# Kernel tuning notes

Hardware: AMD Instinct MI355X
Metric: run time of the kernel (lower is better)

Reference implementation:

```python
import jax, jax.numpy as jnp
import numpy as np

EPS = 1e-6          # RMSNorm eps
SINK_EPS = 1e-12    # Sinkhorn denominator eps
N_ITER = 5          # sinkhorn_iters


def setup_inputs() -> dict:
    key = jax.random.key(0)
    ks = jax.random.split(key, 12)
    B, T, H, D = 2, 2048, 4, 2048
    FD = H * D
    W_SCALE = 0.02  # keep gate logits in a non-saturated sigmoid range
    return {
        "x": jax.random.normal(ks[0], (B, T, H, D), jnp.float32),
        "norm_w": jnp.ones((FD,), jnp.float32),
        "w_pre": jax.random.normal(ks[1], (H, FD), jnp.float32) * W_SCALE,
        "w_res": jax.random.normal(ks[2], (H * H, FD), jnp.float32) * W_SCALE,
        "w_post": jax.random.normal(ks[3], (H, FD), jnp.float32) * W_SCALE,
        "alpha_pre": jax.random.uniform(ks[4], (1,), jnp.float32),
        "alpha_res": jax.random.uniform(ks[5], (1,), jnp.float32),
        "alpha_post": jax.random.uniform(ks[6], (1,), jnp.float32),
        "s_pre": jax.random.normal(ks[7], (H,), jnp.float32),
        "s_res": jax.random.normal(ks[8], (H, H), jnp.float32),
        "s_post": jax.random.normal(ks[9], (H,), jnp.float32),
        "w_inner": jax.random.normal(ks[10], (D, D), jnp.float32) * (1.0 / np.sqrt(D)),
    }


def sinkhorn_knopp(logits, n_iter):
    # Doubly-stochastic projection over last two dims.
    m = jnp.exp(logits - jnp.max(logits, axis=(-2, -1), keepdims=True))
    for _ in range(n_iter):
        m = m / (jnp.sum(m, axis=-1, keepdims=True) + SINK_EPS)
        m = m / (jnp.sum(m, axis=-2, keepdims=True) + SINK_EPS)
    return m


def reference(x, norm_w, w_pre, w_res, w_post, alpha_pre, alpha_res, alpha_post,
              s_pre, s_res, s_post, w_inner):
    b, t, h, d = x.shape
    flat = x.reshape(b, t, h * d)
    # RMSNorm over flat dim
    var = jnp.mean(flat * flat, axis=-1, keepdims=True)
    normed = norm_w * flat * jax.lax.rsqrt(var + EPS)
    # Gate projections (Linear, no bias => x @ W.T)
    a_raw = alpha_pre * (normed @ w_pre.T) + s_pre                     # (b,t,h)
    b_raw = (alpha_res * (normed @ w_res.T)).reshape(b, t, h, h) + s_res
    c_raw = alpha_post * (normed @ w_post.T) + s_post                  # (b,t,h)
    a_l = jax.nn.sigmoid(a_raw)
    c_l = 2.0 * jax.nn.sigmoid(c_raw)
    b_l = sinkhorn_knopp(b_raw, N_ITER)
    # split: inner input
    inner_in = jnp.einsum('bth,bthd->btd', a_l, x)
    # inner layer: bias-free linear
    inner_out = inner_in @ w_inner.T
    # combine
    carry = jnp.einsum('bthk,btkd->bthd', b_l, x)
    write = jnp.einsum('bth,btd->bthd', c_l, inner_out)
    return carry + write
```

## Files before the change

### kernel.cpp

```cpp
#include <hip/hip_runtime.h>
#include <hip/hip_bf16.h>

#define FD 8192
#define DD 2048
#define NH 4
#define NT 4096
#define NG 24
#define NGP 32
#define KSPLIT 32
#define KC (FD / KSPLIT)
#define CH 64

typedef __attribute__((ext_vector_type(4))) float f32x4;
typedef __attribute__((ext_vector_type(8))) short short8;

__device__ inline unsigned short f2bf(float f) {
  __hip_bfloat16 h = __float2bfloat16(f);
  unsigned short u; __builtin_memcpy(&u, &h, 2); return u;
}
__device__ inline float bf2f(unsigned short u) {
  __hip_bfloat16 h; __builtin_memcpy(&h, &u, 2); return __bfloat162float(h);
}

__global__ __launch_bounds__(256) void k_prep(
    const float* __restrict__ w_inner,
    const float* __restrict__ w_pre,
    const float* __restrict__ w_res,
    const float* __restrict__ w_post,
    const float* __restrict__ norm_w,
    unsigned short* __restrict__ w_inner_bf,
    unsigned short* __restrict__ wnb)
{
  const int tid = threadIdx.x;
  const int wid = blockIdx.x * 256 + tid;
  f32x4 w4[4];
#pragma unroll
  for (int it = 0; it < 4; ++it) w4[it] = *(const f32x4*)&w_inner[wid * 16 + it * 4];
  __builtin_amdgcn_sched_barrier(0);
#pragma unroll
  for (int p = 0; p < 2; ++p) {
    f32x4 a = w4[2 * p], b = w4[2 * p + 1];
    short8 o;
    o[0] = (short)f2bf(a.x); o[1] = (short)f2bf(a.y);
    o[2] = (short)f2bf(a.z); o[3] = (short)f2bf(a.w);
    o[4] = (short)f2bf(b.x); o[5] = (short)f2bf(b.y);
    o[6] = (short)f2bf(b.z); o[7] = (short)f2bf(b.w);
    *(short8*)&w_inner_bf[wid * 16 + p * 8] = o;
  }
  {
    int j = wid >> 13, k = wid & (FD - 1);
    float w = (j < 4) ? w_pre[j * FD + k]
            : (j < 20) ? w_res[(j - 4) * FD + k]
            : (j < 24) ? w_post[(j - 20) * FD + k]
            : 0.0f;
    wnb[wid] = f2bf(w * norm_w[k]);
  }
}

__global__ __launch_bounds__(256) void k_gates(
    const float* __restrict__ x, const unsigned short* __restrict__ wnb,
    float* __restrict__ partial ,
    unsigned short* __restrict__ xb )
{
  __shared__ unsigned short xs[128][72];
  const int tb = blockIdx.x;
  const int ks = blockIdx.y;
  const int tid = threadIdx.x;
  const int wave = tid >> 6, lane = tid & 63;
  const int lr = lane & 15, kg = lane >> 4;
  const int t0 = tb * 128;
  const int k0 = ks * KC;
  const int sr = tid >> 4;
  const int sc = (tid & 15) * 4;

  float ssq8[8];
#pragma unroll
  for (int i = 0; i < 8; ++i) ssq8[i] = 0.f;
  f32x4 acc[2][2] = {};

  for (int ch = 0; ch < KC; ch += CH) {
    f32x4 v[8];
#pragma unroll
    for (int it = 0; it < 8; ++it)
      v[it] = *(const f32x4*)&x[(size_t)(t0 + it * 16 + sr) * FD + k0 + ch + sc];
    __builtin_amdgcn_sched_barrier(0);
    __syncthreads();
#pragma unroll
    for (int it = 0; it < 8; ++it) {
      f32x4 a = v[it];
      ssq8[it] += a.x * a.x + a.y * a.y + a.z * a.z + a.w * a.w;
      ushort4 o;
      o.x = f2bf(a.x); o.y = f2bf(a.y); o.z = f2bf(a.z); o.w = f2bf(a.w);
      int r = it * 16 + sr;
      *(ushort4*)&xs[r][sc] = o;
      *(ushort4*)&xb[(size_t)(t0 + r) * FD + k0 + ch + sc] = o;
    }
    __syncthreads();
#pragma unroll
    for (int kk = 0; kk < CH; kk += 32) {
      short8 a2[2], b2[2];
#pragma unroll
      for (int m = 0; m < 2; ++m)
        a2[m] = *(const short8*)&xs[wave * 32 + m * 16 + lr][kk + kg * 8];
#pragma unroll
      for (int n = 0; n < 2; ++n)
        b2[n] = *(const short8*)&wnb[(size_t)(n * 16 + lr) * FD + k0 + ch + kk + kg * 8];
#pragma unroll
      for (int m = 0; m < 2; ++m)
#pragma unroll
        for (int n = 0; n < 2; ++n)
          acc[m][n] = __builtin_amdgcn_mfma_f32_16x16x32_bf16(a2[m], b2[n], acc[m][n], 0, 0, 0);
    }
  }

  float* base = &partial[(size_t)ks * NT * (NG + 1)];
#pragma unroll
  for (int m = 0; m < 2; ++m)
#pragma unroll
    for (int n = 0; n < 2; ++n) {
      int g = n * 16 + lr;
      if (g < NG) {
#pragma unroll
        for (int r = 0; r < 4; ++r) {
          int row = wave * 32 + m * 16 + kg * 4 + r;
          base[(size_t)(t0 + row) * (NG + 1) + g] = acc[m][n][r];
        }
      }
    }
#pragma unroll
  for (int it = 0; it < 8; ++it) {
    float v = ssq8[it];
    v += __shfl_xor(v, 1);
    v += __shfl_xor(v, 2);
    v += __shfl_xor(v, 4);
    v += __shfl_xor(v, 8);
    if ((tid & 15) == 0) {
      int row = it * 16 + sr;
      base[(size_t)(t0 + row) * (NG + 1) + NG] = v;
    }
  }
}

__global__ __launch_bounds__(256) void k_scalars(
    const float* __restrict__ partial,
    const float* __restrict__ alpha_pre, const float* __restrict__ alpha_res,
    const float* __restrict__ alpha_post,
    const float* __restrict__ s_pre, const float* __restrict__ s_res,
    const float* __restrict__ s_post,
    float* __restrict__ gates )
{
  int t = blockIdx.x * blockDim.x + threadIdx.x;
  if (t >= NT) return;
  float acc[NG + 1];
#pragma unroll
  for (int j = 0; j <= NG; ++j) acc[j] = 0.f;
  for (int s = 0; s < KSPLIT; ++s) {
    const float* p = &partial[((size_t)s * NT + t) * (NG + 1)];
#pragma unroll
    for (int j = 0; j <= NG; ++j) acc[j] += p[j];
  }
  float rinv = rsqrtf(acc[NG] * (1.0f / FD) + 1e-6f);
  float ap = alpha_pre[0], ar = alpha_res[0], apo = alpha_post[0];

  float out[NG];
#pragma unroll
  for (int h = 0; h < 4; ++h)
    out[h] = 1.f / (1.f + expf(-(ap * rinv * acc[h] + s_pre[h])));
#pragma unroll
  for (int h = 0; h < 4; ++h)
    out[4 + h] = 2.f / (1.f + expf(-(apo * rinv * acc[20 + h] + s_post[h])));

  float m[16]; float mx = -1e30f;
#pragma unroll
  for (int j = 0; j < 16; ++j) {
    float br = ar * rinv * acc[4 + j] + s_res[j];
    m[j] = br; mx = fmaxf(mx, br);
  }
#pragma unroll
  for (int j = 0; j < 16; ++j) m[j] = expf(m[j] - mx);
#pragma unroll
  for (int it = 0; it < 5; ++it) {
#pragma unroll
    for (int h = 0; h < 4; ++h) {
      float rs = m[h*4] + m[h*4+1] + m[h*4+2] + m[h*4+3];
      float inv = 1.f / (rs + 1e-12f);
      m[h*4] *= inv; m[h*4+1] *= inv; m[h*4+2] *= inv; m[h*4+3] *= inv;
    }
#pragma unroll
    for (int k = 0; k < 4; ++k) {
      float cs = m[k] + m[4+k] + m[8+k] + m[12+k];
      float inv = 1.f / (cs + 1e-12f);
      m[k] *= inv; m[4+k] *= inv; m[8+k] *= inv; m[12+k] *= inv;
    }
  }
#pragma unroll
  for (int j = 0; j < 16; ++j) out[8 + j] = m[j];

  float* gt = &gates[(size_t)t * 24];
#pragma unroll
  for (int j = 0; j < NG; ++j) gt[j] = out[j];
}

__global__ __launch_bounds__(256) void k_inner_in(
    const unsigned short* __restrict__ xb, const float* __restrict__ gates,
    unsigned short* __restrict__ inner_in)
{
  int t = blockIdx.x, tid = threadIdx.x;
  const float* g = &gates[(size_t)t * 24];
  float a0 = g[0], a1 = g[1], a2 = g[2], a3 = g[3];
  const unsigned short* xt = &xb[(size_t)t * FD];
  int d = tid * 8;
  short8 h0 = *(const short8*)&xt[0 * DD + d];
  short8 h1 = *(const short8*)&xt[1 * DD + d];
  short8 h2 = *(const short8*)&xt[2 * DD + d];
  short8 h3 = *(const short8*)&xt[3 * DD + d];
  short8 o;
#pragma unroll
  for (int j = 0; j < 8; ++j) {
    float s = a0 * bf2f((unsigned short)h0[j]) + a1 * bf2f((unsigned short)h1[j])
            + a2 * bf2f((unsigned short)h2[j]) + a3 * bf2f((unsigned short)h3[j]);
    o[j] = (short)f2bf(s);
  }
  *(short8*)&inner_in[(size_t)t * DD + d] = o;
}

__global__ __launch_bounds__(256) void k_gemm(
    const unsigned short* __restrict__ A,
    const unsigned short* __restrict__ B,
    unsigned short* __restrict__ C)
{
  __shared__ unsigned short As[128 * 64];
  __shared__ unsigned short Bs[128 * 64];
  const int bid = blockIdx.x;
  const int bm = bid >> 4, bn = bid & 15;
  const int tid = threadIdx.x;
  const int wave = tid >> 6, lane = tid & 63;
  const int wm = wave >> 1, wn_ = wave & 1;
  const int lr = lane & 15, kg = lane >> 4;

  const int srow = tid >> 3;
  const int scol = (tid & 7) * 8;
  const unsigned short* a_src = &A[(size_t)(bm * 128 + srow) * 2048 + scol];
  const unsigned short* b_src = &B[(size_t)(bn * 128 + srow) * 2048 + scol];

  f32x4 acc[4][4] = {};

  for (int kt = 0; kt < 2048; kt += 64) {
    __syncthreads();
#pragma unroll
    for (int it = 0; it < 4; ++it)
      __builtin_amdgcn_global_load_lds(
          (const __attribute__((address_space(1))) void*)(a_src + (size_t)it * 32 * 2048 + kt),
          (__attribute__((address_space(3))) void*)(&As[it * 2048 + tid * 8]), 16, 0, 0);
#pragma unroll
    for (int it = 0; it < 4; ++it)
      __builtin_amdgcn_global_load_lds(
          (const __attribute__((address_space(1))) void*)(b_src + (size_t)it * 32 * 2048 + kt),
          (__attribute__((address_space(3))) void*)(&Bs[it * 2048 + tid * 8]), 16, 0, 0);
    __syncthreads();
#pragma unroll
    for (int kk = 0; kk < 64; kk += 32) {
      short8 a[4], b[4];
#pragma unroll
      for (int m = 0; m < 4; ++m)
        a[m] = *(const short8*)&As[(wm * 64 + m * 16 + lr) * 64 + kk + kg * 8];
#pragma unroll
      for (int n = 0; n < 4; ++n)
        b[n] = *(const short8*)&Bs[(wn_ * 64 + n * 16 + lr) * 64 + kk + kg * 8];
#pragma unroll
      for (int m = 0; m < 4; ++m)
#pragma unroll
        for (int n = 0; n < 4; ++n)
          acc[m][n] = __builtin_amdgcn_mfma_f32_16x16x32_bf16(a[m], b[n], acc[m][n], 0, 0, 0);
    }
  }

  const int row_base = bm * 128 + wm * 64;
  const int col_base = bn * 128 + wn_ * 64;
#pragma unroll
  for (int m = 0; m < 4; ++m)
#pragma unroll
    for (int n = 0; n < 4; ++n) {
      int col = col_base + n * 16 + lr;
#pragma unroll
      for (int r = 0; r < 4; ++r) {
        int row = row_base + m * 16 + kg * 4 + r;
        C[(size_t)row * 2048 + col] = f2bf(acc[m][n][r]);
      }
    }
}

__global__ __launch_bounds__(256) void k_out(
    const unsigned short* __restrict__ xb, const float* __restrict__ gates,
    const unsigned short* __restrict__ inner_out, float* __restrict__ out)
{
  int t = blockIdx.x, tid = threadIdx.x;
  const float* g = &gates[(size_t)t * 24];
  float c[4], bl[16];
#pragma unroll
  for (int h = 0; h < 4; ++h) c[h] = g[4 + h];
#pragma unroll
  for (int j = 0; j < 16; ++j) bl[j] = g[8 + j];
  const unsigned short* xt = &xb[(size_t)t * FD];
  float* ot = &out[(size_t)t * FD];
  int d = tid * 8;
  short8 xh[4];
#pragma unroll
  for (int h = 0; h < 4; ++h) xh[h] = *(const short8*)&xt[h * DD + d];
  short8 iu = *(const short8*)&inner_out[(size_t)t * DD + d];
  float io[8], xf[4][8];
#pragma unroll
  for (int j = 0; j < 8; ++j) io[j] = bf2f((unsigned short)iu[j]);
#pragma unroll
  for (int h = 0; h < 4; ++h)
#pragma unroll
    for (int j = 0; j < 8; ++j) xf[h][j] = bf2f((unsigned short)xh[h][j]);
#pragma unroll
  for (int h = 0; h < 4; ++h) {
    f32x4 o0, o1;
#pragma unroll
    for (int j = 0; j < 4; ++j) {
      o0[j] = c[h] * io[j]     + bl[h*4+0] * xf[0][j]     + bl[h*4+1] * xf[1][j]
                               + bl[h*4+2] * xf[2][j]     + bl[h*4+3] * xf[3][j];
      o1[j] = c[h] * io[j + 4] + bl[h*4+0] * xf[0][j + 4] + bl[h*4+1] * xf[1][j + 4]
                               + bl[h*4+2] * xf[2][j + 4] + bl[h*4+3] * xf[3][j + 4];
    }
    *(f32x4*)&ot[h * DD + d] = o0;
    *(f32x4*)&ot[h * DD + d + 4] = o1;
  }
}

extern "C" void kernel_launch(void* const* d_in, const int* in_sizes, int n_in,
                              void* d_out, int out_size, void* d_ws, size_t ws_size,
                              hipStream_t stream) {
  const float* x          = (const float*)d_in[0];
  const float* norm_w     = (const float*)d_in[1];
  const float* w_pre      = (const float*)d_in[2];
  const float* w_res      = (const float*)d_in[3];
  const float* w_post     = (const float*)d_in[4];
  const float* alpha_pre  = (const float*)d_in[5];
  const float* alpha_res  = (const float*)d_in[6];
  const float* alpha_post = (const float*)d_in[7];
  const float* s_pre      = (const float*)d_in[8];
  const float* s_res      = (const float*)d_in[9];
  const float* s_post     = (const float*)d_in[10];
  const float* w_inner    = (const float*)d_in[11];
  float* out = (float*)d_out;

  char* ws = (char*)d_ws;
  size_t off = 0;
  auto alloc = [&](size_t bytes) -> void* {
    void* p = ws + off;
    off = (off + bytes + 255) & ~(size_t)255;
    return p;
  };
  unsigned short* w_inner_bf = (unsigned short*)alloc((size_t)DD * DD * 2);
  unsigned short* inner_in   = (unsigned short*)alloc((size_t)NT * DD * 2);
  unsigned short* inner_out  = (unsigned short*)alloc((size_t)NT * DD * 2);
  unsigned short* wnb        = (unsigned short*)alloc((size_t)NGP * FD * 2);
  unsigned short* xb         = (unsigned short*)alloc((size_t)NT * FD * 2);
  float* partial = (float*)alloc((size_t)KSPLIT * NT * (NG + 1) * 4);
  float* gates   = (float*)alloc((size_t)NT * 24 * 4);

  k_prep<<<1024, 256, 0, stream>>>(w_inner, w_pre, w_res, w_post, norm_w, w_inner_bf, wnb);
  k_gates<<<dim3(32, 32), 256, 0, stream>>>(x, wnb, partial, xb);
  k_scalars<<<16, 256, 0, stream>>>(partial, alpha_pre, alpha_res, alpha_post,
                                    s_pre, s_res, s_post, gates);
  k_inner_in<<<4096, 256, 0, stream>>>(xb, gates, inner_in);
  k_gemm<<<512, 256, 0, stream>>>(inner_in, w_inner_bf, inner_out);
  k_out<<<4096, 256, 0, stream>>>(xb, gates, inner_out, out);
}
```

Baseline: 173.9 us.

## Fuse gate scalar reduction into inner_in kernel and widen gates K-chunk

Merges the per-token partial-sum reduction, sigmoid and Sinkhorn gate computation with the inner_in weighted sum in one kernel, one block per token. This removes a separate launch, and the old reduction kernel ran only 16 blocks with serial per-thread loops. It also doubles the k_gates chunk to 128 columns with 8-wide vector loads and stores and adds a minimum-occupancy launch bound. The cost is extra shared memory and registers in k_gates, and a serial single-thread gate computation inside each fused block.

```diff
diff --git a/kernel.cpp b/kernel.cpp
--- a/kernel.cpp
+++ b/kernel.cpp
@@ -9,7 +9,7 @@
 #define NGP 32
 #define KSPLIT 32
 #define KC (FD / KSPLIT)
-#define CH 64
+#define CH 128
 
 typedef __attribute__((ext_vector_type(4))) float f32x4;
 typedef __attribute__((ext_vector_type(8))) short short8;
@@ -57,12 +57,12 @@
   }
 }
 
-__global__ __launch_bounds__(256) void k_gates(
+__global__ __launch_bounds__(256, 4) void k_gates(
     const float* __restrict__ x, const unsigned short* __restrict__ wnb,
     float* __restrict__ partial ,
     unsigned short* __restrict__ xb )
 {
-  __shared__ unsigned short xs[128][72];
+  __shared__ unsigned short xs[128][136];
   const int tb = blockIdx.x;
   const int ks = blockIdx.y;
   const int tid = threadIdx.x;
@@ -71,7 +71,7 @@
   const int t0 = tb * 128;
   const int k0 = ks * KC;
   const int sr = tid >> 4;
-  const int sc = (tid & 15) * 4;
+  const int sc = (tid & 15) * 8;
 
   float ssq8[8];
 #pragma unroll
@@ -79,21 +79,28 @@
   f32x4 acc[2][2] = {};
 
   for (int ch = 0; ch < KC; ch += CH) {
-    f32x4 v[8];
-#pragma unroll
-    for (int it = 0; it < 8; ++it)
-      v[it] = *(const f32x4*)&x[(size_t)(t0 + it * 16 + sr) * FD + k0 + ch + sc];
+    f32x4 v[16];
+#pragma unroll
+    for (int it = 0; it < 8; ++it) {
+      size_t goff = (size_t)(t0 + it * 16 + sr) * FD + k0 + ch + sc;
+      v[2 * it]     = *(const f32x4*)&x[goff];
+      v[2 * it + 1] = *(const f32x4*)&x[goff + 4];
+    }
     __builtin_amdgcn_sched_barrier(0);
     __syncthreads();
 #pragma unroll
     for (int it = 0; it < 8; ++it) {
-      f32x4 a = v[it];
-      ssq8[it] += a.x * a.x + a.y * a.y + a.z * a.z + a.w * a.w;
-      ushort4 o;
-      o.x = f2bf(a.x); o.y = f2bf(a.y); o.z = f2bf(a.z); o.w = f2bf(a.w);
+      f32x4 a = v[2 * it], b = v[2 * it + 1];
+      ssq8[it] += a.x * a.x + a.y * a.y + a.z * a.z + a.w * a.w
+                + b.x * b.x + b.y * b.y + b.z * b.z + b.w * b.w;
+      short8 o;
+      o[0] = (short)f2bf(a.x); o[1] = (short)f2bf(a.y);
+      o[2] = (short)f2bf(a.z); o[3] = (short)f2bf(a.w);
+      o[4] = (short)f2bf(b.x); o[5] = (short)f2bf(b.y);
+      o[6] = (short)f2bf(b.z); o[7] = (short)f2bf(b.w);
       int r = it * 16 + sr;
-      *(ushort4*)&xs[r][sc] = o;
-      *(ushort4*)&xb[(size_t)(t0 + r) * FD + k0 + ch + sc] = o;
+      *(short8*)&xs[r][sc] = o;
+      *(short8*)&xb[(size_t)(t0 + r) * FD + k0 + ch + sc] = o;
     }
     __syncthreads();
 #pragma unroll
@@ -141,73 +148,79 @@
   }
 }
 
-__global__ __launch_bounds__(256) void k_scalars(
+__global__ __launch_bounds__(256) void k_fuse(
     const float* __restrict__ partial,
+    const unsigned short* __restrict__ xb,
     const float* __restrict__ alpha_pre, const float* __restrict__ alpha_res,
     const float* __restrict__ alpha_post,
     const float* __restrict__ s_pre, const float* __restrict__ s_res,
     const float* __restrict__ s_post,
-    float* __restrict__ gates )
-{
-  int t = blockIdx.x * blockDim.x + threadIdx.x;
-  if (t >= NT) return;
-  float acc[NG + 1];
-#pragma unroll
-  for (int j = 0; j <= NG; ++j) acc[j] = 0.f;
-  for (int s = 0; s < KSPLIT; ++s) {
-    const float* p = &partial[((size_t)s * NT + t) * (NG + 1)];
-#pragma unroll
-    for (int j = 0; j <= NG; ++j) acc[j] += p[j];
-  }
-  float rinv = rsqrtf(acc[NG] * (1.0f / FD) + 1e-6f);
-  float ap = alpha_pre[0], ar = alpha_res[0], apo = alpha_post[0];
-
-  float out[NG];
-#pragma unroll
-  for (int h = 0; h < 4; ++h)
-    out[h] = 1.f / (1.f + expf(-(ap * rinv * acc[h] + s_pre[h])));
-#pragma unroll
-  for (int h = 0; h < 4; ++h)
-    out[4 + h] = 2.f / (1.f + expf(-(apo * rinv * acc[20 + h] + s_post[h])));
-
-  float m[16]; float mx = -1e30f;
-#pragma unroll
-  for (int j = 0; j < 16; ++j) {
-    float br = ar * rinv * acc[4 + j] + s_res[j];
-    m[j] = br; mx = fmaxf(mx, br);
-  }
-#pragma unroll
-  for (int j = 0; j < 16; ++j) m[j] = expf(m[j] - mx);
-#pragma unroll
-  for (int it = 0; it < 5; ++it) {
-#pragma unroll
-    for (int h = 0; h < 4; ++h) {
-      float rs = m[h*4] + m[h*4+1] + m[h*4+2] + m[h*4+3];
-      float inv = 1.f / (rs + 1e-12f);
-      m[h*4] *= inv; m[h*4+1] *= inv; m[h*4+2] *= inv; m[h*4+3] *= inv;
-    }
-#pragma unroll
-    for (int k = 0; k < 4; ++k) {
-      float cs = m[k] + m[4+k] + m[8+k] + m[12+k];
-      float inv = 1.f / (cs + 1e-12f);
-      m[k] *= inv; m[4+k] *= inv; m[8+k] *= inv; m[12+k] *= inv;
-    }
-  }
-#pragma unroll
-  for (int j = 0; j < 16; ++j) out[8 + j] = m[j];
-
-  float* gt = &gates[(size_t)t * 24];
-#pragma unroll
-  for (int j = 0; j < NG; ++j) gt[j] = out[j];
-}
-
-__global__ __launch_bounds__(256) void k_inner_in(
-    const unsigned short* __restrict__ xb, const float* __restrict__ gates,
+    float* __restrict__ gates ,
     unsigned short* __restrict__ inner_in)
 {
-  int t = blockIdx.x, tid = threadIdx.x;
-  const float* g = &gates[(size_t)t * 24];
-  float a0 = g[0], a1 = g[1], a2 = g[2], a3 = g[3];
+  const int t = blockIdx.x, tid = threadIdx.x;
+  __shared__ float sred[8][NG + 1];
+  __shared__ float sacc[NG + 1];
+  __shared__ float sg[4];
+
+  if (tid < 8 * (NG + 1)) {
+    int j = tid % (NG + 1), grp = tid / (NG + 1);
+    float a = 0.f;
+#pragma unroll
+    for (int s = 0; s < 4; ++s)
+      a += partial[((size_t)(grp * 4 + s) * NT + t) * (NG + 1) + j];
+    sred[grp][j] = a;
+  }
+  __syncthreads();
+  if (tid < NG + 1) {
+    float a = 0.f;
+#pragma unroll
+    for (int i = 0; i < 8; ++i) a += sred[i][tid];
+    sacc[tid] = a;
+  }
+  __syncthreads();
+  if (tid == 0) {
+    float rinv = rsqrtf(sacc[NG] * (1.0f / FD) + 1e-6f);
+    float ap = alpha_pre[0], ar = alpha_res[0], apo = alpha_post[0];
+    float out[NG];
+#pragma unroll
+    for (int h = 0; h < 4; ++h)
+      out[h] = 1.f / (1.f + expf(-(ap * rinv * sacc[h] + s_pre[h])));
+#pragma unroll
+    for (int h = 0; h < 4; ++h)
+      out[4 + h] = 2.f / (1.f + expf(-(apo * rinv * sacc[20 + h] + s_post[h])));
+    float m[16]; float mx = -1e30f;
+#pragma unroll
+    for (int j = 0; j < 16; ++j) {
+      float br = ar * rinv * sacc[4 + j] + s_res[j];
+      m[j] = br; mx = fmaxf(mx, br);
+    }
+#pragma unroll
+    for (int j = 0; j < 16; ++j) m[j] = expf(m[j] - mx);
+#pragma unroll
+    for (int it = 0; it < 5; ++it) {
+#pragma unroll
+      for (int h = 0; h < 4; ++h) {
+        float rs = m[h*4] + m[h*4+1] + m[h*4+2] + m[h*4+3];
+        float inv = 1.f / (rs + 1e-12f);
+        m[h*4] *= inv; m[h*4+1] *= inv; m[h*4+2] *= inv; m[h*4+3] *= inv;
+      }
+#pragma unroll
+      for (int k = 0; k < 4; ++k) {
+        float cs = m[k] + m[4+k] + m[8+k] + m[12+k];
+        float inv = 1.f / (cs + 1e-12f);
+        m[k] *= inv; m[4+k] *= inv; m[8+k] *= inv; m[12+k] *= inv;
+      }
+    }
+#pragma unroll
+    for (int j = 0; j < 16; ++j) out[8 + j] = m[j];
+    float* gt = &gates[(size_t)t * 24];
+#pragma unroll
+    for (int j = 0; j < NG; ++j) gt[j] = out[j];
+    sg[0] = out[0]; sg[1] = out[1]; sg[2] = out[2]; sg[3] = out[3];
+  }
+  __syncthreads();
+  float a0 = sg[0], a1 = sg[1], a2 = sg[2], a3 = sg[3];
   const unsigned short* xt = &xb[(size_t)t * FD];
   int d = tid * 8;
   short8 h0 = *(const short8*)&xt[0 * DD + d];
@@ -364,9 +377,8 @@
 
   k_prep<<<1024, 256, 0, stream>>>(w_inner, w_pre, w_res, w_post, norm_w, w_inner_bf, wnb);
   k_gates<<<dim3(32, 32), 256, 0, stream>>>(x, wnb, partial, xb);
-  k_scalars<<<16, 256, 0, stream>>>(partial, alpha_pre, alpha_res, alpha_post,
-                                    s_pre, s_res, s_post, gates);
-  k_inner_in<<<4096, 256, 0, stream>>>(xb, gates, inner_in);
+  k_fuse<<<4096, 256, 0, stream>>>(partial, xb, alpha_pre, alpha_res, alpha_post,
+                                   s_pre, s_res, s_post, gates, inner_in);
   k_gemm<<<512, 256, 0, stream>>>(inner_in, w_inner_bf, inner_out);
   k_out<<<4096, 256, 0, stream>>>(xb, gates, inner_out, out);
 }
```

Result: slower. 213.1 us (+22.6%).
